# Performance work log

Hardware: AMD Instinct MI355X
Metric: run time of the kernel (lower is better)

The kernel has to match this reference:

```python
import jax, jax.numpy as jnp
import numpy as np

B, T, H, F = 16, 2048, 256, 1024


def lstm_layer(x, Wih, Whh, b):
    """PyTorch-convention LSTM layer. x: [B,T,Hin], Wih: [4H,Hin], Whh: [4H,H], b: [4H].
    Gate order i, f, g, o (as in torch.nn.LSTM). Returns hidden seq [B,T,H]."""
    bsz = x.shape[0]
    hid = Whh.shape[1]
    # precompute input contribution for all timesteps (one big GEMM)
    xg = jnp.einsum('bti,gi->btg', x, Wih) + b  # [B,T,4H]

    def step(carry, xt):
        h, c = carry
        gates = xt + h @ Whh.T  # [B,4H]
        i, f, g, o = jnp.split(gates, 4, axis=-1)
        i = jax.nn.sigmoid(i)
        f = jax.nn.sigmoid(f)
        g = jnp.tanh(g)
        o = jax.nn.sigmoid(o)
        c = f * c + i * g
        h = o * jnp.tanh(c)
        return (h, c), h

    h0 = jnp.zeros((bsz, hid), x.dtype)
    (_, _), hs = jax.lax.scan(step, (h0, h0), jnp.swapaxes(xg, 0, 1))  # [T,B,H]
    return jnp.swapaxes(hs, 0, 1)


def setup_inputs() -> dict:
    key = jax.random.key(0)
    ks = jax.random.split(key, 13)
    s = jnp.float32(0.05)  # small weight scale to keep gates in their linear-ish regime
    return {
        'x': jax.random.uniform(ks[0], (B, T, H), jnp.float32),
        'lstm0_Wih': jax.random.normal(ks[1], (4, 4 * H, H), jnp.float32) * s,
        'lstm0_Whh': jax.random.normal(ks[2], (4, 4 * H, H), jnp.float32) * s,
        'lstm0_b': jax.random.normal(ks[3], (4, 4 * H), jnp.float32) * s,
        'fo_W': jax.random.normal(ks[4], (F, H), jnp.float32) * s,
        'fo_b': jax.random.normal(ks[5], (F,), jnp.float32) * s,
        'fi_W': jax.random.normal(ks[6], (H, F), jnp.float32) * s,
        'fi_b': jax.random.normal(ks[7], (H,), jnp.float32) * s,
        'lstm1_Wih': jax.random.normal(ks[8], (4 * H, H), jnp.float32) * s,
        'lstm1_Whh': jax.random.normal(ks[9], (4 * H, H), jnp.float32) * s,
        'lstm1_b': jax.random.normal(ks[10], (4 * H,), jnp.float32) * s,
        'head_W': jax.random.normal(ks[11], (1, H), jnp.float32) * s,
        'head_b': jax.random.normal(ks[12], (1,), jnp.float32) * s,
    }


def reference(x, lstm0_Wih, lstm0_Whh, lstm0_b, fo_W, fo_b, fi_W, fi_b,
              lstm1_Wih, lstm1_Whh, lstm1_b, head_W, head_b):
    h = x
    # 4-layer stacked LSTM (zero init state, as torch default)
    for l in range(lstm0_Wih.shape[0]):
        h = lstm_layer(h, lstm0_Wih[l], lstm0_Whh[l], lstm0_b[l])
    # fan_out -> LeakyReLU(0.2) -> fan_in
    h = h @ fo_W.T + fo_b
    h = jnp.where(h >= 0, h, 0.2 * h)
    h = h @ fi_W.T + fi_b
    # single-layer LSTM
    h = lstm_layer(h, lstm1_Wih, lstm1_Whh, lstm1_b)
    # output head on last timestep, sigmoid
    logits = h[:, -1, :] @ head_W.T + head_b  # [B,1]
    return jax.nn.sigmoid(logits[:, 0])
```

## Files before the change

### kernel.cpp

```cpp
#include <hip/hip_runtime.h>
#include <stdint.h>


#define B_ 16
#define T_ 2048
#define H_ 256
#define NG 1024
#define F_ 1024
#define CHUNK 8
#define NCH 256
#define WH 128
#define WXG 128
#define WCH 16
#define PREC 4
#define NRECB 20
#define NBLK 56
#define APITCH 264
#define WELEM 262144

typedef __attribute__((ext_vector_type(4))) float f32x4;
typedef __attribute__((ext_vector_type(8))) short bf16x8;
typedef unsigned long long ull;

#define OFF_XG   0ul
#define SZ_XG    (5ul*WXG*NG*B_*4ul)
#define OFF_H    (OFF_XG + SZ_XG)
#define SZ_H     (5ul*WH*B_*H_*2ul)
#define OFF_FO   (OFF_H + SZ_H)
#define SZ_FO    ((unsigned long)WCH*128ul*F_*2ul)
#define OFF_FI   (OFF_FO + SZ_FO)
#define SZ_FI    ((unsigned long)WCH*128ul*H_*2ul)
#define OFF_WBF  (OFF_FI + SZ_FI)
#define SZ_WBF   (7ul*WELEM*2ul)
#define OFF_H4   (OFF_WBF + SZ_WBF)
#define OFF_FLAG (OFF_H4 + 16384ul + 256ul)

#define FL_PF(l,p) ((((l)*4)+(p))*16)
#define FL_XGF(s)  (320 + (s)*16)
#define FL_FOF     400
#define FL_FIF     416
#define FL_XGP(s)  (432 + (s)*4)
#define FL_FOP     452
#define FL_FIP     460
#define FL_N       512

#define BAR() do { asm volatile("" ::: "memory"); \
                   __builtin_amdgcn_s_barrier(); \
                   asm volatile("" ::: "memory"); } while (0)

__device__ __forceinline__ unsigned short f2bf(float f) {
  unsigned int u = __float_as_uint(f);
  u = u + 0x7fffu + ((u >> 16) & 1u);
  return (unsigned short)(u >> 16);
}
__device__ __forceinline__ float sigm_f(float x) { return 1.0f / (1.0f + __expf(-x)); }
__device__ __forceinline__ float tanh_f(float x) {
  float e = __expf(-2.0f * fabsf(x));
  float r = (1.0f - e) / (1.0f + e);
  return x >= 0.0f ? r : -r;
}
__device__ __forceinline__ unsigned ld32(const void* p) {
  return __hip_atomic_load((const unsigned*)p, __ATOMIC_RELAXED, __HIP_MEMORY_SCOPE_AGENT);
}
__device__ __forceinline__ void st32(void* p, unsigned v) {
  __hip_atomic_store((unsigned*)p, v, __ATOMIC_RELAXED, __HIP_MEMORY_SCOPE_AGENT);
}
__device__ __forceinline__ ull ld64(const void* p) {
  return __hip_atomic_load((const ull*)p, __ATOMIC_RELAXED, __HIP_MEMORY_SCOPE_AGENT);
}
__device__ __forceinline__ void st64(void* p, ull v) {
  __hip_atomic_store((ull*)p, v, __ATOMIC_RELAXED, __HIP_MEMORY_SCOPE_AGENT);
}
__device__ __forceinline__ void spin_ge(unsigned int* p, unsigned int tgt) {
  int n = 0;
  while (ld32(p) < tgt) {
    __builtin_amdgcn_s_sleep(1);
    if (++n > 20000000) break;
  }
}
__device__ __forceinline__ void spin_tight(unsigned int* p, unsigned int tgt) {
  int n = 0;
  while (ld32(p) < tgt) {
    if (++n > 200000) break;
  }
}

__global__ void k_prep(const float* __restrict__ w0ih, const float* __restrict__ w1ih,
                       const float* __restrict__ foW, const float* __restrict__ fiW,
                       unsigned char* ws) {
  unsigned short* wbf = (unsigned short*)(ws + OFF_WBF);
  unsigned int* flags = (unsigned int*)(ws + OFF_FLAG);
  if (blockIdx.x == 0) {
    for (int i = threadIdx.x; i < FL_N; i += 256) flags[i] = 0u;
  }
  int gid = blockIdx.x * 256 + threadIdx.x;
  if (gid < 7 * WELEM) {
    int which = gid >> 18;
    int idx = gid & (WELEM - 1);
    float v;
    if (which < 4)       v = w0ih[(size_t)which * WELEM + idx];
    else if (which == 4) v = w1ih[idx];
    else if (which == 5) v = foW[idx];
    else                 v = fiW[idx];
    wbf[gid] = f2bf(v);
  }
}

#define ISSUE_XA(TT, DST) do { \
    const ull* xg8_ = (const ull*)(xg_ring + ((size_t)l * WXG + (size_t)((TT) & 127)) * (NG * B_)); \
    _Pragma("unroll") \
    for (int g_ = 0; g_ < 4; ++g_) { \
      size_t n8_ = (size_t)(g_ * 256 + unit) * 8 + quad * 2; \
      DST[g_][0] = ld64(xg8_ + n8_); \
      DST[g_][1] = ld64(xg8_ + n8_ + 1); \
    } \
  } while (0)

#define REC_STEP(T, CB, XC, XN) do { \
    const int t_ = (T); \
    if ((t_ & 7) == 0) { \
      int tc_ = t_ >> 3; \
      if (wave == 0) { \
        unsigned int* wp_ = (unsigned int*)0; unsigned wt_ = 0u; \
        if (lane == 0) { wp_ = xgf + (tc_ & 15); wt_ = (unsigned)(tc_ + 1); }   \
        else if (l < 4 && tc_ >= WCH) {                                         \
          unsigned g_ = (unsigned)(tc_ - WCH + 1); \
          if (l < 3) { if (lane >= 1 && lane <= 4) { wp_ = flags + FL_XGP(l + 1) + (lane - 1); wt_ = g_; } } \
          else       { if (lane >= 1 && lane <= 8) { wp_ = flags + FL_FOP + (lane - 1); wt_ = g_; } } \
        } \
        if (wp_) spin_ge(wp_, wt_); \
      } \
      BAR(); \
      ISSUE_XA(t_, XC); \
    } \
     \
    f32x4 ac_[4]; \
    _Pragma("unroll") for (int g_ = 0; g_ < 4; ++g_) ac_[g_] = (f32x4){0.f, 0.f, 0.f, 0.f}; \
    _Pragma("unroll") \
    for (int kk_ = 0; kk_ < 8; ++kk_) { \
      bf16x8 af_ = *(const bf16x8*)(&smem[(CB) * 16 * APITCH + c16 * APITCH + kk_ * 32 + quad * 8]); \
      _Pragma("unroll") \
      for (int g_ = 0; g_ < 4; ++g_) \
        ac_[g_] = __builtin_amdgcn_mfma_f32_16x16x32_bf16(af_, bfr[g_][kk_], ac_[g_], 0, 0, 0); \
    } \
     \
    float hv_[4]; \
    _Pragma("unroll") \
    for (int r_ = 0; r_ < 4; ++r_) { \
      union { ull u; float f[2]; } u0_, u1_, u2_, u3_; \
      u0_.u = XC[0][r_ >> 1]; u1_.u = XC[1][r_ >> 1]; \
      u2_.u = XC[2][r_ >> 1]; u3_.u = XC[3][r_ >> 1]; \
      float iv_ = sigm_f(ac_[0][r_] + u0_.f[r_ & 1]); \
      float fv_ = sigm_f(ac_[1][r_] + u1_.f[r_ & 1]); \
      float gv_ = tanh_f(ac_[2][r_] + u2_.f[r_ & 1]); \
      float ov_ = sigm_f(ac_[3][r_] + u3_.f[r_ & 1]); \
      cst[r_] = fv_ * cst[r_] + iv_ * gv_; \
      hv_[r_] = ov_ * tanh_f(cst[r_]); \
      if (l == 4 && t_ == T_ - 1) h4_last[(quad * 4 + r_) * H_ + unit] = hv_[r_]; \
    } \
     \
    unsigned pk_[4]; \
    _Pragma("unroll") \
    for (int r_ = 0; r_ < 4; ++r_) { \
      float oth_ = __shfl_xor(hv_[r_], 1, 64); \
      pk_[r_] = (unsigned)f2bf(hv_[r_]) | ((unsigned)f2bf(oth_) << 16); \
    } \
     \
    { unsigned short* hrw_ = h_ring + ((size_t)l * WH + (size_t)(t_ & 127)) * (B_ * H_); \
      if ((lane & 1) == 0) { \
        _Pragma("unroll") \
        for (int r_ = 0; r_ < 4; ++r_) \
          st32(hrw_ + (size_t)(quad * 4 + r_) * H_ + unit, pk_[r_]); \
      } } \
    asm volatile("" ::: "memory");           \
    if ((t_ & 7) != 7) ISSUE_XA(t_ + 1, XN);    \
     \
    if ((lane & 1) == 0) { \
      _Pragma("unroll") \
      for (int r_ = 0; r_ < 4; ++r_) \
        *(unsigned*)&smem[(((CB) ^ 1) * 16 + (quad * 4 + r_)) * APITCH + unit] = pk_[r_]; \
    } \
     \
    if ((t_ & 7) != 7) { asm volatile("s_waitcnt vmcnt(8)" ::: "memory"); } \
    else               { asm volatile("s_waitcnt vmcnt(0)" ::: "memory"); } \
    BAR();                                    \
    if (tid == 0) st32(mypf, (unsigned)(t_ + 1)); \
     \
    if (wave < 3) { \
      int fp_ = (p + 1 + wave) & 3; \
      spin_tight(flags + FL_PF(l, fp_), (unsigned)(t_ + 1)); \
      int b2_ = lane >> 2, q4_ = lane & 3; \
      const ull* src8_ = (const ull*)(h_ring + ((size_t)l * WH + (size_t)(t_ & 127)) * (B_ * H_) + \
                                      (size_t)b2_ * H_ + fp_ * 64 + q4_ * 16); \
      ull v0_ = ld64(src8_ + 0), v1_ = ld64(src8_ + 1); \
      ull v2_ = ld64(src8_ + 2), v3_ = ld64(src8_ + 3); \
      ull* dst8_ = (ull*)&smem[(((CB) ^ 1) * 16 + b2_) * APITCH + fp_ * 64 + q4_ * 16]; \
      dst8_[0] = v0_; dst8_[1] = v1_; dst8_[2] = v2_; dst8_[3] = v3_; \
    } \
    asm volatile("s_waitcnt lgkmcnt(0)" ::: "memory"); \
    BAR();                                    \
  } while (0)

__global__ __launch_bounds__(256, 1) void k_pipe(
    const float* __restrict__ x,
    const float* __restrict__ w0hh, const float* __restrict__ b0,
    const float* __restrict__ fo_b, const float* __restrict__ fi_b,
    const float* __restrict__ w1hh, const float* __restrict__ b1,
    unsigned char* ws)
{
  __shared__ unsigned short smem[64 * APITCH];

  float*          xg_ring = (float*)(ws + OFF_XG);
  unsigned short* h_ring  = (unsigned short*)(ws + OFF_H);
  unsigned short* fo_ring = (unsigned short*)(ws + OFF_FO);
  unsigned short* fi_ring = (unsigned short*)(ws + OFF_FI);
  unsigned short* wbf     = (unsigned short*)(ws + OFF_WBF);
  float*          h4_last = (float*)(ws + OFF_H4);
  unsigned int*   flags   = (unsigned int*)(ws + OFF_FLAG);

  const int tid = threadIdx.x;
  const int lane = tid & 63;
  const int wave = tid >> 6;
  const int quad = lane >> 4;
  const int c16 = lane & 15;
  const int bid = blockIdx.x;

  if (bid < NRECB) {
    const int l = bid / PREC, p = bid % PREC;
    const int unit = (p * 4 + wave) * 16 + c16;
    const float* Whh = (l < 4) ? (w0hh + (size_t)l * NG * H_) : w1hh;

    bf16x8 bfr[4][8];
#pragma unroll
    for (int g = 0; g < 4; ++g) {
      const float* rp = Whh + (size_t)(g * 256 + unit) * H_ + quad * 8;
#pragma unroll
      for (int kk = 0; kk < 8; ++kk) {
        const float* q = rp + kk * 32;
        bf16x8 pk;
#pragma unroll
        for (int jj = 0; jj < 8; ++jj) pk[jj] = (short)f2bf(q[jj]);
        bfr[g][kk] = pk;
      }
    }
    for (int i = tid; i < 2 * 16 * APITCH; i += 256) smem[i] = 0;
    float cst[4] = {0.f, 0.f, 0.f, 0.f};
    __syncthreads();

    unsigned int* xgf  = flags + FL_XGF(l);
    unsigned int* mypf = flags + FL_PF(l, p);

    ull xaA[4][2], xaB[4][2];
    for (int t2 = 0; t2 < T_; t2 += 2) {
      REC_STEP(t2,     0, xaA, xaB);
      REC_STEP(t2 + 1, 1, xaB, xaA);
    }
  } else {
    int sb = bid - NRECB, s, j, GSS;
    if (sb < 20)      { s = sb >> 2; j = sb & 3;  GSS = 4; }
    else if (sb < 28) { s = 5;       j = sb - 20; GSS = 8; }
    else              { s = 6;       j = sb - 28; GSS = 8; }
    const bool isXG = (s < 5), isFO = (s == 5), isFI = (s == 6);
    const unsigned short* Bw = wbf + (size_t)(isXG ? s : (isFO ? 5 : 6)) * WELEM;
    const float* bias = isXG ? ((s < 4) ? (b0 + s * NG) : b1) : (isFO ? fo_b : fi_b);
    unsigned int* myprog =
        flags + (isXG ? (FL_XGP(s) + j) : (isFO ? (FL_FOP + j) : (FL_FIP + j)));

    for (int tc = j; tc < NCH; tc += GSS) {
      if (tc >= WCH) {
        unsigned int tgt = (unsigned)(tc - WCH + 1);
        if (isXG)      { if (tid < 4) spin_ge(flags + FL_PF(s, tid), 8u * tgt); }
        else if (isFO) { if (tid < 8) spin_ge(flags + FL_FIP + tid, tgt); }
        else           { if (tid < 4) spin_ge(flags + FL_XGP(4) + tid, tgt); }
      }
      if (isXG) {
        if (s >= 1 && s <= 3) { if (tid < 4) spin_ge(flags + FL_PF(s - 1, tid), 8u * (unsigned)(tc + 1)); }
        else if (s == 4)      { if (tid == 0) spin_ge(flags + FL_FIF + (tc & 15), (unsigned)(tc + 1)); }
      } else if (isFO) {
        if (tid < 4) spin_ge(flags + FL_PF(3, tid), 8u * (unsigned)(tc + 1));
      } else {
        if (tid == 0) spin_ge(flags + FL_FOF + (tc & 15), (unsigned)(tc + 1));
      }
      __syncthreads();

      if (!isFI) {
#pragma unroll
        for (int m_blk = 0; m_blk < 2; ++m_blk) {
          __syncthreads();
          {
            int rloc = tid >> 2;
            int k0 = (tid & 3) * 64;
            int row = m_blk * 64 + rloc;
            int tl = row >> 4, b = row & 15;
            int t = tc * CHUNK + tl;
            unsigned short* dst = &smem[rloc * APITCH + k0];
            if (s == 0) {
              const float* src = x + ((size_t)b * T_ + t) * H_ + k0;
#pragma unroll
              for (int i = 0; i < 16; ++i) {
                f32x4 v = *(const f32x4*)(src + i * 4);
                *(unsigned*)(dst + i * 4)     = (unsigned)f2bf(v[0]) | ((unsigned)f2bf(v[1]) << 16);
                *(unsigned*)(dst + i * 4 + 2) = (unsigned)f2bf(v[2]) | ((unsigned)f2bf(v[3]) << 16);
              }
            } else {
              const unsigned short* src;
              if (isXG && s <= 3)
                src = h_ring + ((size_t)(s - 1) * WH + (size_t)(t & 127)) * (B_ * H_) + b * H_ + k0;
              else if (isXG)
                src = fi_ring + ((size_t)(tc & 15) * 128 + row) * H_ + k0;
              else
                src = h_ring + ((size_t)3 * WH + (size_t)(t & 127)) * (B_ * H_) + b * H_ + k0;
#pragma unroll
              for (int i = 0; i < 16; ++i)
                *(ull*)(dst + i * 4) = ld64((const ull*)src + i);
            }
          }
          __syncthreads();
          bf16x8 afr[4][8];
#pragma unroll
          for (int mt = 0; mt < 4; ++mt)
#pragma unroll
            for (int kk = 0; kk < 8; ++kk)
              afr[mt][kk] = *(const bf16x8*)(&smem[(mt * 16 + c16) * APITCH + kk * 32 + quad * 8]);
          for (int nn = 0; nn < 16; ++nn) {
            int n = (wave * 16 + nn) * 16 + c16;
            const unsigned short* bp = Bw + (size_t)n * 256 + quad * 8;
            bf16x8 bfr2[8];
#pragma unroll
            for (int kk = 0; kk < 8; ++kk) bfr2[kk] = *(const bf16x8*)(bp + kk * 32);
            f32x4 ac[4];
#pragma unroll
            for (int mt = 0; mt < 4; ++mt) ac[mt] = (f32x4){0.f, 0.f, 0.f, 0.f};
#pragma unroll
            for (int kk = 0; kk < 8; ++kk)
#pragma unroll
              for (int mt = 0; mt < 4; ++mt)
                ac[mt] = __builtin_amdgcn_mfma_f32_16x16x32_bf16(afr[mt][kk], bfr2[kk], ac[mt], 0, 0, 0);
            float bn = bias[n];
            if (isXG) {
              ull* xg8 = (ull*)(xg_ring + (size_t)s * WXG * (NG * B_));
#pragma unroll
              for (int mt = 0; mt < 4; ++mt) {
                int t = tc * CHUNK + m_blk * 4 + mt;
                size_t bi = ((size_t)(t & 127) * (NG * B_) + (size_t)n * B_ + quad * 4) >> 1;
                union { ull u; float f[2]; } u0, u1;
                u0.f[0] = ac[mt][0] + bn; u0.f[1] = ac[mt][1] + bn;
                u1.f[0] = ac[mt][2] + bn; u1.f[1] = ac[mt][3] + bn;
                st64(xg8 + bi, u0.u);
                st64(xg8 + bi + 1, u1.u);
              }
            } else {
#pragma unroll
              for (int mt = 0; mt < 4; ++mt) {
                int row = m_blk * 64 + mt * 16 + quad * 4;
#pragma unroll
                for (int r = 0; r < 4; ++r) {
                  float v = ac[mt][r] + bn;
                  v = v >= 0.f ? v : 0.2f * v;
                  float oth = __shfl_xor(v, 1, 64);
                  if ((lane & 1) == 0) {
                    unsigned pk = (unsigned)f2bf(v) | ((unsigned)f2bf(oth) << 16);
                    st32(fo_ring + ((size_t)(tc & 15) * 128 + row + r) * F_ + n, pk);
                  }
                }
              }
            }
          }
        }
      } else {
        f32x4 acc[2][4][4];
#pragma unroll
        for (int a1 = 0; a1 < 2; ++a1)
#pragma unroll
          for (int a2 = 0; a2 < 4; ++a2)
#pragma unroll
            for (int a3 = 0; a3 < 4; ++a3) acc[a1][a2][a3] = (f32x4){0.f, 0.f, 0.f, 0.f};
#pragma unroll
        for (int ks = 0; ks < 4; ++ks) {
#pragma unroll
          for (int m_blk = 0; m_blk < 2; ++m_blk) {
            __syncthreads();
            {
              int rloc = tid >> 2;
              int k0 = (tid & 3) * 64;
              int row = m_blk * 64 + rloc;
              const unsigned short* src =
                  fo_ring + ((size_t)(tc & 15) * 128 + row) * F_ + ks * 256 + k0;
              unsigned short* dst = &smem[rloc * APITCH + k0];
#pragma unroll
              for (int i = 0; i < 16; ++i)
                *(ull*)(dst + i * 4) = ld64((const ull*)src + i);
            }
            __syncthreads();
            bf16x8 afr[4][8];
#pragma unroll
            for (int mt = 0; mt < 4; ++mt)
#pragma unroll
              for (int kk = 0; kk < 8; ++kk)
                afr[mt][kk] = *(const bf16x8*)(&smem[(mt * 16 + c16) * APITCH + kk * 32 + quad * 8]);
#pragma unroll
            for (int nn = 0; nn < 4; ++nn) {
              int n = (wave * 4 + nn) * 16 + c16;
              const unsigned short* bp = Bw + (size_t)n * 1024 + ks * 256 + quad * 8;
              bf16x8 bfr2[8];
#pragma unroll
              for (int kk = 0; kk < 8; ++kk) bfr2[kk] = *(const bf16x8*)(bp + kk * 32);
#pragma unroll
              for (int kk = 0; kk < 8; ++kk)
#pragma unroll
                for (int mt = 0; mt < 4; ++mt)
                  acc[m_blk][nn][mt] =
                      __builtin_amdgcn_mfma_f32_16x16x32_bf16(afr[mt][kk], bfr2[kk], acc[m_blk][nn][mt], 0, 0, 0);
            }
          }
        }
#pragma unroll
        for (int m_blk = 0; m_blk < 2; ++m_blk)
#pragma unroll
          for (int nn = 0; nn < 4; ++nn) {
            int n = (wave * 4 + nn) * 16 + c16;
            float bn = bias[n];
#pragma unroll
            for (int mt = 0; mt < 4; ++mt) {
              int row = m_blk * 64 + mt * 16 + quad * 4;
#pragma unroll
              for (int r = 0; r < 4; ++r) {
                float v = acc[m_blk][nn][mt][r] + bn;
                float oth = __shfl_xor(v, 1, 64);
                if ((lane & 1) == 0) {
                  unsigned pk = (unsigned)f2bf(v) | ((unsigned)f2bf(oth) << 16);
                  st32(fi_ring + ((size_t)(tc & 15) * 128 + row + r) * H_ + n, pk);
                }
              }
            }
          }
      }
      __syncthreads();
      if (tid == 0) {
        unsigned int* fl = isXG ? (flags + FL_XGF(s) + (tc & 15))
                                : (isFO ? (flags + FL_FOF + (tc & 15)) : (flags + FL_FIF + (tc & 15)));
        st32(fl, (unsigned)(tc + 1));
        st32(myprog, (unsigned)(tc + 1));
      }
    }
  }
}

__global__ void k_head(const float* __restrict__ hW, const float* __restrict__ hb,
                       unsigned char* ws, float* __restrict__ out) {
  __shared__ float red[256];
  const float* h4 = (const float*)(ws + OFF_H4);
  int tid = threadIdx.x;
  int b = tid >> 4, k0 = tid & 15;
  float sum = 0.f;
  for (int k = k0; k < H_; k += 16) sum += h4[b * H_ + k] * hW[k];
  red[tid] = sum;
  __syncthreads();
  if (tid < B_) {
    float z = hb[0];
    for (int i = 0; i < 16; ++i) z += red[tid * 16 + i];
    out[tid] = 1.0f / (1.0f + __expf(-z));
  }
}

extern "C" void kernel_launch(void* const* d_in, const int* in_sizes, int n_in,
                              void* d_out, int out_size, void* d_ws, size_t ws_size,
                              hipStream_t stream) {
  const float* x    = (const float*)d_in[0];
  const float* w0ih = (const float*)d_in[1];
  const float* w0hh = (const float*)d_in[2];
  const float* b0   = (const float*)d_in[3];
  const float* foW  = (const float*)d_in[4];
  const float* fob  = (const float*)d_in[5];
  const float* fiW  = (const float*)d_in[6];
  const float* fib  = (const float*)d_in[7];
  const float* w1ih = (const float*)d_in[8];
  const float* w1hh = (const float*)d_in[9];
  const float* b1   = (const float*)d_in[10];
  const float* hW   = (const float*)d_in[11];
  const float* hb   = (const float*)d_in[12];
  unsigned char* ws = (unsigned char*)d_ws;
  (void)in_sizes; (void)n_in; (void)out_size; (void)ws_size;

  hipLaunchKernelGGL(k_prep, dim3(7168), dim3(256), 0, stream, w0ih, w1ih, foW, fiW, ws);
  hipLaunchKernelGGL(k_pipe, dim3(NBLK), dim3(256), 0, stream,
                     x, w0hh, b0, fob, fib, w1hh, b1, ws);
  hipLaunchKernelGGL(k_head, dim3(1), dim3(256), 0, stream, hW, hb, ws, (float*)d_out);
}
```

Baseline: 6.063 ms.

## Replace per-step flag barrier with tagged-data exchange ring for hidden-state sharing

Each recurrent block now also writes its packed bf16 hidden values, each tagged with the timestep, into a small exchange ring. Peer blocks poll those tagged words directly instead of waiting on a block barrier, a flag store and a flag spin before loading. This removes one block barrier and the flag publish/acquire round trip from every serial timestep, and keeps the per-block flag only every 8 steps for downstream consumers. It costs doubled store traffic and spinning on 8 loads per lane, and relies on the 64-bit tagged stores being seen atomically.

```diff
diff --git a/kernel.cpp b/kernel.cpp
--- a/kernel.cpp
+++ b/kernel.cpp
@@ -34,6 +34,8 @@
 #define SZ_WBF   (7ul*WELEM*2ul)
 #define OFF_H4   (OFF_WBF + SZ_WBF)
 #define OFF_FLAG (OFF_H4 + 16384ul + 256ul)
+#define OFF_EX   (OFF_FLAG + 4096ul)
+#define N_EXQ    (5*8*4*16*32)
 
 #define FL_PF(l,p) ((((l)*4)+(p))*16)
 #define FL_XGF(s)  (320 + (s)*16)
@@ -78,12 +80,6 @@
     if (++n > 20000000) break;
   }
 }
-__device__ __forceinline__ void spin_tight(unsigned int* p, unsigned int tgt) {
-  int n = 0;
-  while (ld32(p) < tgt) {
-    if (++n > 200000) break;
-  }
-}
 
 __global__ void k_prep(const float* __restrict__ w0ih, const float* __restrict__ w1ih,
                        const float* __restrict__ foW, const float* __restrict__ fiW,
@@ -92,6 +88,11 @@
   unsigned int* flags = (unsigned int*)(ws + OFF_FLAG);
   if (blockIdx.x == 0) {
     for (int i = threadIdx.x; i < FL_N; i += 256) flags[i] = 0u;
+  }
+  if (blockIdx.x >= 8 && blockIdx.x < 48) {
+    ull* ex = (ull*)(ws + OFF_EX);
+    int base = (blockIdx.x - 8) * 2048;
+    for (int i = threadIdx.x; i < 2048; i += 256) ex[base + i] = 0ull;
   }
   int gid = blockIdx.x * 256 + threadIdx.x;
   if (gid < 7 * WELEM) {
@@ -167,10 +168,15 @@
     } \
      \
     { unsigned short* hrw_ = h_ring + ((size_t)l * WH + (size_t)(t_ & 127)) * (B_ * H_); \
+      ull* exw_ = ex_ring + (((size_t)l * 8 + (size_t)(t_ & 7)) * 4 + p) * (16 * 32); \
       if ((lane & 1) == 0) { \
+        int lp_ = (unit - p * 64) >> 1; \
+        ull tagw_ = ((ull)(unsigned)(t_ + 1)) << 32; \
         _Pragma("unroll") \
-        for (int r_ = 0; r_ < 4; ++r_) \
+        for (int r_ = 0; r_ < 4; ++r_) { \
           st32(hrw_ + (size_t)(quad * 4 + r_) * H_ + unit, pk_[r_]); \
+          st64(exw_ + (size_t)(quad * 4 + r_) * 32 + lp_, (ull)pk_[r_] | tagw_); \
+        } \
       } } \
     asm volatile("" ::: "memory");           \
     if ((t_ & 7) != 7) ISSUE_XA(t_ + 1, XN);    \
@@ -181,24 +187,30 @@
         *(unsigned*)&smem[(((CB) ^ 1) * 16 + (quad * 4 + r_)) * APITCH + unit] = pk_[r_]; \
     } \
      \
-    if ((t_ & 7) != 7) { asm volatile("s_waitcnt vmcnt(8)" ::: "memory"); } \
-    else               { asm volatile("s_waitcnt vmcnt(0)" ::: "memory"); } \
-    BAR();                                    \
-    if (tid == 0) st32(mypf, (unsigned)(t_ + 1)); \
-     \
     if (wave < 3) { \
       int fp_ = (p + 1 + wave) & 3; \
-      spin_tight(flags + FL_PF(l, fp_), (unsigned)(t_ + 1)); \
-      int b2_ = lane >> 2, q4_ = lane & 3; \
-      const ull* src8_ = (const ull*)(h_ring + ((size_t)l * WH + (size_t)(t_ & 127)) * (B_ * H_) + \
-                                      (size_t)b2_ * H_ + fp_ * 64 + q4_ * 16); \
-      ull v0_ = ld64(src8_ + 0), v1_ = ld64(src8_ + 1); \
-      ull v2_ = ld64(src8_ + 2), v3_ = ld64(src8_ + 3); \
-      ull* dst8_ = (ull*)&smem[(((CB) ^ 1) * 16 + b2_) * APITCH + fp_ * 64 + q4_ * 16]; \
-      dst8_[0] = v0_; dst8_[1] = v1_; dst8_[2] = v2_; dst8_[3] = v3_; \
-    } \
+      const ull* src_ = ex_ring + ((((size_t)l * 8 + (size_t)(t_ & 7)) * 4 + fp_) * 16 + (lane >> 2)) * 32 + \
+                        (size_t)(lane & 3) * 8; \
+      unsigned tg_ = (unsigned)(t_ + 1); \
+      ull g_[8]; \
+      int it_ = 0; \
+      while (true) { \
+        _Pragma("unroll") \
+        for (int j_ = 0; j_ < 8; ++j_) g_[j_] = ld64(src_ + j_); \
+        bool ok_ = true; \
+        _Pragma("unroll") \
+        for (int j_ = 0; j_ < 8; ++j_) ok_ = ok_ && ((unsigned)(g_[j_] >> 32) == tg_); \
+        if (ok_ || ++it_ > 5000) break; \
+      } \
+      ull* dst_ = (ull*)&smem[(((CB) ^ 1) * 16 + (lane >> 2)) * APITCH + fp_ * 64 + (lane & 3) * 16]; \
+      _Pragma("unroll") \
+      for (int j_ = 0; j_ < 4; ++j_) \
+        dst_[j_] = ((ull)(unsigned)g_[2 * j_]) | (((ull)(unsigned)g_[2 * j_ + 1]) << 32); \
+    } \
+    if ((t_ & 7) == 7) { asm volatile("s_waitcnt vmcnt(0)" ::: "memory"); }   \
     asm volatile("s_waitcnt lgkmcnt(0)" ::: "memory"); \
     BAR();                                    \
+    if ((t_ & 7) == 7) { if (tid == 0) st32(mypf, (unsigned)(t_ + 1)); }      \
   } while (0)
 
 __global__ __launch_bounds__(256, 1) void k_pipe(
@@ -217,6 +229,7 @@
   unsigned short* wbf     = (unsigned short*)(ws + OFF_WBF);
   float*          h4_last = (float*)(ws + OFF_H4);
   unsigned int*   flags   = (unsigned int*)(ws + OFF_FLAG);
+  ull*            ex_ring = (ull*)(ws + OFF_EX);
 
   const int tid = threadIdx.x;
   const int lane = tid & 63;
```

Result: slower. 6.780 ms (+11.8%).

## Replace hidden-state ring with timestep-tagged exchange to skip flag waits

Applied to the files above, without the earlier changes.

Hidden-state outputs are now written as 64-bit words carrying the packed bf16 pair plus a timestep tag, into a new zero-initialised exchange buffer. Consumers in both the recurrent blocks and the GEMM stages poll the data itself and check the tags, so they no longer wait on vmcnt drains or partner flags on the common path. This removes a store-to-flag round trip from each step's critical path. In exchange the buffer doubles in size, extra traffic is needed to zero it, consumers spin on data with retry loops, and the spin timeout is raised.

```diff
diff --git a/kernel.cpp b/kernel.cpp
--- a/kernel.cpp
+++ b/kernel.cpp
@@ -9,7 +9,6 @@
 #define F_ 1024
 #define CHUNK 8
 #define NCH 256
-#define WH 128
 #define WXG 128
 #define WCH 16
 #define PREC 4
@@ -24,9 +23,10 @@
 
 #define OFF_XG   0ul
 #define SZ_XG    (5ul*WXG*NG*B_*4ul)
-#define OFF_H    (OFF_XG + SZ_XG)
-#define SZ_H     (5ul*WH*B_*H_*2ul)
-#define OFF_FO   (OFF_H + SZ_H)
+#define OFF_TEX  (OFF_XG + SZ_XG)
+#define N_TEX    (5ul*128ul*16ul*128ul)
+#define SZ_TEX   (N_TEX*8ul)
+#define OFF_FO   (OFF_TEX + SZ_TEX)
 #define SZ_FO    ((unsigned long)WCH*128ul*F_*2ul)
 #define OFF_FI   (OFF_FO + SZ_FO)
 #define SZ_FI    ((unsigned long)WCH*128ul*H_*2ul)
@@ -81,7 +81,7 @@
 __device__ __forceinline__ void spin_tight(unsigned int* p, unsigned int tgt) {
   int n = 0;
   while (ld32(p) < tgt) {
-    if (++n > 200000) break;
+    if (++n > 1000000) break;
   }
 }
 
@@ -93,10 +93,12 @@
   if (blockIdx.x == 0) {
     for (int i = threadIdx.x; i < FL_N; i += 256) flags[i] = 0u;
   }
-  int gid = blockIdx.x * 256 + threadIdx.x;
+  size_t gid = (size_t)blockIdx.x * 256 + threadIdx.x;
+  ull* tex = (ull*)(ws + OFF_TEX);
+  for (size_t i = gid; i < N_TEX; i += (size_t)gridDim.x * 256) tex[i] = 0ull;
   if (gid < 7 * WELEM) {
-    int which = gid >> 18;
-    int idx = gid & (WELEM - 1);
+    int which = (int)(gid >> 18);
+    int idx = (int)(gid & (WELEM - 1));
     float v;
     if (which < 4)       v = w0ih[(size_t)which * WELEM + idx];
     else if (which == 4) v = w1ih[idx];
@@ -166,13 +168,15 @@
       pk_[r_] = (unsigned)f2bf(hv_[r_]) | ((unsigned)f2bf(oth_) << 16); \
     } \
      \
-    { unsigned short* hrw_ = h_ring + ((size_t)l * WH + (size_t)(t_ & 127)) * (B_ * H_); \
-      if ((lane & 1) == 0) { \
-        _Pragma("unroll") \
-        for (int r_ = 0; r_ < 4; ++r_) \
-          st32(hrw_ + (size_t)(quad * 4 + r_) * H_ + unit, pk_[r_]); \
-      } } \
-    asm volatile("" ::: "memory");           \
+    if ((lane & 1) == 0) { \
+      ull tagw_ = ((ull)(unsigned)(t_ + 1)) << 32; \
+      ull* exw_ = tex + ((size_t)l * 128 + (size_t)(t_ & 127)) * (16 * 128); \
+      int gg_ = unit >> 1; \
+      _Pragma("unroll") \
+      for (int r_ = 0; r_ < 4; ++r_) \
+        st64(exw_ + (size_t)(quad * 4 + r_) * 128 + gg_, (ull)pk_[r_] | tagw_); \
+    } \
+    asm volatile("" ::: "memory"); \
     if ((t_ & 7) != 7) ISSUE_XA(t_ + 1, XN);    \
      \
     if ((lane & 1) == 0) { \
@@ -180,22 +184,31 @@
       for (int r_ = 0; r_ < 4; ++r_) \
         *(unsigned*)&smem[(((CB) ^ 1) * 16 + (quad * 4 + r_)) * APITCH + unit] = pk_[r_]; \
     } \
-     \
-    if ((t_ & 7) != 7) { asm volatile("s_waitcnt vmcnt(8)" ::: "memory"); } \
-    else               { asm volatile("s_waitcnt vmcnt(0)" ::: "memory"); } \
     BAR();                                    \
-    if (tid == 0) st32(mypf, (unsigned)(t_ + 1)); \
+    if (tid == 0) st32(mypf, (unsigned)(t_ + 1));    \
      \
     if (wave < 3) { \
       int fp_ = (p + 1 + wave) & 3; \
-      spin_tight(flags + FL_PF(l, fp_), (unsigned)(t_ + 1)); \
-      int b2_ = lane >> 2, q4_ = lane & 3; \
-      const ull* src8_ = (const ull*)(h_ring + ((size_t)l * WH + (size_t)(t_ & 127)) * (B_ * H_) + \
-                                      (size_t)b2_ * H_ + fp_ * 64 + q4_ * 16); \
-      ull v0_ = ld64(src8_ + 0), v1_ = ld64(src8_ + 1); \
-      ull v2_ = ld64(src8_ + 2), v3_ = ld64(src8_ + 3); \
-      ull* dst8_ = (ull*)&smem[(((CB) ^ 1) * 16 + b2_) * APITCH + fp_ * 64 + q4_ * 16]; \
-      dst8_[0] = v0_; dst8_[1] = v1_; dst8_[2] = v2_; dst8_[3] = v3_; \
+      unsigned tg_ = (unsigned)(t_ + 1); \
+      const ull* src_ = tex + (((size_t)l * 128 + (size_t)(t_ & 127)) * 16 + (lane >> 2)) * 128 + \
+                        fp_ * 32 + (lane & 3) * 8; \
+      ull g_[8]; \
+      _Pragma("unroll") for (int j_ = 0; j_ < 8; ++j_) g_[j_] = ld64(src_ + j_); \
+      bool ok_ = true; \
+      _Pragma("unroll") for (int j_ = 0; j_ < 8; ++j_) ok_ = ok_ && ((unsigned)(g_[j_] >> 32) == tg_); \
+      if (!ok_) { \
+        spin_tight(flags + FL_PF(l, fp_), tg_);    \
+        int it_ = 0; \
+        do { \
+          _Pragma("unroll") for (int j_ = 0; j_ < 8; ++j_) g_[j_] = ld64(src_ + j_); \
+          ok_ = true; \
+          _Pragma("unroll") for (int j_ = 0; j_ < 8; ++j_) ok_ = ok_ && ((unsigned)(g_[j_] >> 32) == tg_); \
+        } while (!ok_ && ++it_ < 100000); \
+      } \
+      ull* dst_ = (ull*)&smem[(((CB) ^ 1) * 16 + (lane >> 2)) * APITCH + fp_ * 64 + (lane & 3) * 16]; \
+      _Pragma("unroll") \
+      for (int j_ = 0; j_ < 4; ++j_) \
+        dst_[j_] = ((ull)(unsigned)g_[2 * j_]) | (((ull)(unsigned)g_[2 * j_ + 1]) << 32); \
     } \
     asm volatile("s_waitcnt lgkmcnt(0)" ::: "memory"); \
     BAR();                                    \
@@ -211,7 +224,7 @@
   __shared__ unsigned short smem[64 * APITCH];
 
   float*          xg_ring = (float*)(ws + OFF_XG);
-  unsigned short* h_ring  = (unsigned short*)(ws + OFF_H);
+  ull*            tex     = (ull*)(ws + OFF_TEX);
   unsigned short* fo_ring = (unsigned short*)(ws + OFF_FO);
   unsigned short* fi_ring = (unsigned short*)(ws + OFF_FI);
   unsigned short* wbf     = (unsigned short*)(ws + OFF_WBF);
@@ -302,17 +315,33 @@
                 *(unsigned*)(dst + i * 4)     = (unsigned)f2bf(v[0]) | ((unsigned)f2bf(v[1]) << 16);
                 *(unsigned*)(dst + i * 4 + 2) = (unsigned)f2bf(v[2]) | ((unsigned)f2bf(v[3]) << 16);
               }
-            } else {
-              const unsigned short* src;
-              if (isXG && s <= 3)
-                src = h_ring + ((size_t)(s - 1) * WH + (size_t)(t & 127)) * (B_ * H_) + b * H_ + k0;
-              else if (isXG)
-                src = fi_ring + ((size_t)(tc & 15) * 128 + row) * H_ + k0;
-              else
-                src = h_ring + ((size_t)3 * WH + (size_t)(t & 127)) * (B_ * H_) + b * H_ + k0;
+            } else if (isXG && s == 4) {
+              const unsigned short* src = fi_ring + ((size_t)(tc & 15) * 128 + row) * H_ + k0;
 #pragma unroll
               for (int i = 0; i < 16; ++i)
                 *(ull*)(dst + i * 4) = ld64((const ull*)src + i);
+            } else {
+              int lsrc = isFO ? 3 : (s - 1);
+              unsigned tg = (unsigned)(t + 1);
+              const ull* srcq = tex + (((size_t)lsrc * 128 + (size_t)(t & 127)) * 16 + b) * 128 +
+                                (size_t)(tid & 3) * 32;
+#pragma unroll
+              for (int grp = 0; grp < 4; ++grp) {
+                ull g[8];
+                int it = 0;
+                bool ok;
+                do {
+#pragma unroll
+                  for (int jj = 0; jj < 8; ++jj) g[jj] = ld64(srcq + grp * 8 + jj);
+                  ok = true;
+#pragma unroll
+                  for (int jj = 0; jj < 8; ++jj) ok = ok && ((unsigned)(g[jj] >> 32) == tg);
+                } while (!ok && ++it < 200000);
+                ull* dst8 = (ull*)(dst + grp * 16);
+#pragma unroll
+                for (int jj = 0; jj < 4; ++jj)
+                  dst8[jj] = ((ull)(unsigned)g[2 * jj]) | (((ull)(unsigned)g[2 * jj + 1]) << 32);
+              }
             }
           }
           __syncthreads();
```

Result: slower. 6.383 ms (+5.3%).

## Exchange hidden state via tagged 64-bit slots to skip per-step store drain

Applied to the files above, without the earlier changes.

Each recurrent block now also writes its bf16 hidden-state pairs into a small exchange buffer, packing the timestep number into the upper 32 bits of each 64-bit word. Peer blocks check these tags to confirm the data is valid, so the per-step s_waitcnt vmcnt drain before publishing the flag is removed. A separate early flag (mysf) is still set each step, and the original progress flag is published only every 8 steps after a full drain. The aim is to take global-store completion latency off the serial critical path of the recurrence, at the cost of twice as many bytes exchanged and retry loops on the reads.

```diff
diff --git a/kernel.cpp b/kernel.cpp
--- a/kernel.cpp
+++ b/kernel.cpp
@@ -34,6 +34,8 @@
 #define SZ_WBF   (7ul*WELEM*2ul)
 #define OFF_H4   (OFF_WBF + SZ_WBF)
 #define OFF_FLAG (OFF_H4 + 16384ul + 256ul)
+#define OFF_TEX  (OFF_FLAG + 8192ul)
+#define N_TEX    (5*8*16*128)
 
 #define FL_PF(l,p) ((((l)*4)+(p))*16)
 #define FL_XGF(s)  (320 + (s)*16)
@@ -42,7 +44,8 @@
 #define FL_XGP(s)  (432 + (s)*4)
 #define FL_FOP     452
 #define FL_FIP     460
-#define FL_N       512
+#define FL_SF(l,p) (512 + (((l)*4)+(p))*16)
+#define FL_N       896
 
 #define BAR() do { asm volatile("" ::: "memory"); \
                    __builtin_amdgcn_s_barrier(); \
@@ -92,6 +95,11 @@
   unsigned int* flags = (unsigned int*)(ws + OFF_FLAG);
   if (blockIdx.x == 0) {
     for (int i = threadIdx.x; i < FL_N; i += 256) flags[i] = 0u;
+  }
+  if (blockIdx.x >= 8 && blockIdx.x < 48) {
+    ull* tex = (ull*)(ws + OFF_TEX);
+    int base = (blockIdx.x - 8) * 2048;
+    for (int i = threadIdx.x; i < 2048; i += 256) tex[base + i] = 0ull;
   }
   int gid = blockIdx.x * 256 + threadIdx.x;
   if (gid < 7 * WELEM) {
@@ -167,10 +175,15 @@
     } \
      \
     { unsigned short* hrw_ = h_ring + ((size_t)l * WH + (size_t)(t_ & 127)) * (B_ * H_); \
+      ull* exw_ = tex + ((size_t)l * 8 + (size_t)(t_ & 7)) * (16 * 128); \
       if ((lane & 1) == 0) { \
+        ull tagw_ = ((ull)(unsigned)(t_ + 1)) << 32; \
+        int gg_ = unit >> 1; \
         _Pragma("unroll") \
-        for (int r_ = 0; r_ < 4; ++r_) \
+        for (int r_ = 0; r_ < 4; ++r_) { \
           st32(hrw_ + (size_t)(quad * 4 + r_) * H_ + unit, pk_[r_]); \
+          st64(exw_ + (size_t)(quad * 4 + r_) * 128 + gg_, (ull)pk_[r_] | tagw_); \
+        } \
       } } \
     asm volatile("" ::: "memory");           \
     if ((t_ & 7) != 7) ISSUE_XA(t_ + 1, XN);    \
@@ -180,25 +193,35 @@
       for (int r_ = 0; r_ < 4; ++r_) \
         *(unsigned*)&smem[(((CB) ^ 1) * 16 + (quad * 4 + r_)) * APITCH + unit] = pk_[r_]; \
     } \
-     \
-    if ((t_ & 7) != 7) { asm volatile("s_waitcnt vmcnt(8)" ::: "memory"); } \
-    else               { asm volatile("s_waitcnt vmcnt(0)" ::: "memory"); } \
     BAR();                                    \
-    if (tid == 0) st32(mypf, (unsigned)(t_ + 1)); \
+    if (tid == 0) st32(mysf, (unsigned)(t_ + 1));    \
      \
     if (wave < 3) { \
       int fp_ = (p + 1 + wave) & 3; \
-      spin_tight(flags + FL_PF(l, fp_), (unsigned)(t_ + 1)); \
-      int b2_ = lane >> 2, q4_ = lane & 3; \
-      const ull* src8_ = (const ull*)(h_ring + ((size_t)l * WH + (size_t)(t_ & 127)) * (B_ * H_) + \
-                                      (size_t)b2_ * H_ + fp_ * 64 + q4_ * 16); \
-      ull v0_ = ld64(src8_ + 0), v1_ = ld64(src8_ + 1); \
-      ull v2_ = ld64(src8_ + 2), v3_ = ld64(src8_ + 3); \
-      ull* dst8_ = (ull*)&smem[(((CB) ^ 1) * 16 + b2_) * APITCH + fp_ * 64 + q4_ * 16]; \
-      dst8_[0] = v0_; dst8_[1] = v1_; dst8_[2] = v2_; dst8_[3] = v3_; \
+      unsigned tg_ = (unsigned)(t_ + 1); \
+      spin_tight(flags + FL_SF(l, fp_), tg_); \
+      const ull* src_ = tex + (((size_t)l * 8 + (size_t)(t_ & 7)) * 16 + (lane >> 2)) * 128 + \
+                        fp_ * 32 + (lane & 3) * 8; \
+      ull g_[8]; \
+      bool ok_; int it_ = 0; \
+      do { \
+        _Pragma("unroll") for (int j_ = 0; j_ < 8; ++j_) g_[j_] = ld64(src_ + j_); \
+        ok_ = true; \
+        _Pragma("unroll") for (int j_ = 0; j_ < 8; ++j_) ok_ = ok_ && ((unsigned)(g_[j_] >> 32) == tg_); \
+      } while (!ok_ && ++it_ < 100000); \
+      ull* dst_ = (ull*)&smem[(((CB) ^ 1) * 16 + (lane >> 2)) * APITCH + fp_ * 64 + (lane & 3) * 16]; \
+      _Pragma("unroll") \
+      for (int j_ = 0; j_ < 4; ++j_) \
+        dst_[j_] = ((ull)(unsigned)g_[2 * j_]) | (((ull)(unsigned)g_[2 * j_ + 1]) << 32); \
     } \
     asm volatile("s_waitcnt lgkmcnt(0)" ::: "memory"); \
     BAR();                                    \
+     \
+    if ((t_ & 7) == 7) { \
+      asm volatile("s_waitcnt vmcnt(0)" ::: "memory"); \
+      BAR(); \
+      if (tid == 0) st32(mypf, (unsigned)(t_ + 1)); \
+    } \
   } while (0)
 
 __global__ __launch_bounds__(256, 1) void k_pipe(
@@ -217,6 +240,7 @@
   unsigned short* wbf     = (unsigned short*)(ws + OFF_WBF);
   float*          h4_last = (float*)(ws + OFF_H4);
   unsigned int*   flags   = (unsigned int*)(ws + OFF_FLAG);
+  ull*            tex     = (ull*)(ws + OFF_TEX);
 
   const int tid = threadIdx.x;
   const int lane = tid & 63;
@@ -249,6 +273,7 @@
 
     unsigned int* xgf  = flags + FL_XGF(l);
     unsigned int* mypf = flags + FL_PF(l, p);
+    unsigned int* mysf = flags + FL_SF(l, p);
 
     ull xaA[4][2], xaB[4][2];
     for (int t2 = 0; t2 < T_; t2 += 2) {
```

After: 7.354 ms. 21.3% more time.
